# Performance work log

Measured on AMD Instinct MI355X. Metric: run time of the kernel, lower is better.

Reference implementation:

```python
import jax, jax.numpy as jnp
import numpy as np

WS = 14           # window_size
N = WS * WS       # tokens = 196
DIM = 768
H = 12
HD = DIM // H     # 64
B = 256
KSZ = 3


def make_local_mask():
    # True = masked out; 3x3 neighborhood around each query is kept (False)
    mask = np.ones((N, N), dtype=bool)
    for i in range(WS):
        for j in range(WS):
            cur = np.ones((WS, WS), dtype=bool)
            stx, sty = max(i - KSZ // 2, 0), max(j - KSZ // 2, 0)
            edx, edy = min(i + KSZ // 2, WS - 1), min(j + KSZ // 2, WS - 1)
            cur[stx:edx + 1, sty:edy + 1] = False
            mask[i * WS + j] = cur.reshape(-1)
    return mask


def make_rel_idx():
    coords = np.stack(np.meshgrid(np.arange(WS), np.arange(WS), indexing='ij'))  # [2,WS,WS]
    flat = coords.reshape(2, -1)                                                  # [2,N]
    rel = flat[:, :, None] - flat[:, None, :]                                     # [2,N,N]
    rel = rel.transpose(1, 2, 0).astype(np.int32)                                 # [N,N,2]
    rel[:, :, 0] += WS - 1
    rel[:, :, 1] += WS - 1
    rel[:, :, 0] *= 2 * WS - 1
    return rel.sum(-1)                                                            # [N,N] in [0, (2WS-1)^2)


def setup_inputs() -> dict:
    key = jax.random.key(0)
    ks = jax.random.split(key, 5)
    return {
        'x': jax.random.normal(ks[0], (B, N, DIM), jnp.float32),
        'w_qkv': jax.random.normal(ks[1], (3 * DIM, DIM), jnp.float32) * 0.02,
        'rpb_table': jax.random.normal(ks[2], ((2 * WS - 1) ** 2, H), jnp.float32) * 0.02,
        'proj_w': jax.random.normal(ks[3], (DIM, DIM), jnp.float32) * 0.02,
        'proj_b': jax.random.normal(ks[4], (DIM,), jnp.float32) * 0.02,
        'mask': jnp.asarray(make_local_mask()),
        'rel_idx': jnp.asarray(make_rel_idx()),
    }


def reference(x, w_qkv, rpb_table, proj_w, proj_b, mask, rel_idx):
    b, n, c = x.shape
    scale = HD ** -0.5
    qkv = x @ w_qkv.T                                   # [B,N,3*DIM]
    qkv = qkv.reshape(b, n, 3, H, HD).transpose(2, 0, 3, 1, 4)  # [3,B,H,N,HD]
    q, k, v = qkv[0] * scale, qkv[1], qkv[2]
    attn = jnp.einsum('bhqd,bhkd->bhqk', q, k)          # [B,H,N,N]
    neg = -jnp.finfo(attn.dtype).max
    attn = jnp.where(mask, neg, attn)
    # relative position bias gather: [N,N] indices into [T,H] -> [H,N,N]
    rpb = rpb_table[rel_idx].transpose(2, 0, 1)
    attn = attn + rpb[None]
    attn = jax.nn.softmax(attn, axis=-1)
    out = jnp.einsum('bhqk,bhkd->bhqd', attn, v)        # [B,H,N,HD]
    out = out.transpose(0, 2, 1, 3).reshape(b, n, H * HD)
    return out @ proj_w.T + proj_b
```

## Files before the change

kernel.cpp:

```cpp
#include <hip/hip_runtime.h>
#include <cstdint>
#include <cstddef>

typedef unsigned short u16;
typedef __attribute__((ext_vector_type(8))) short bf16x8;
typedef __attribute__((ext_vector_type(4))) float f32x4;

__device__ __forceinline__ u16 f2bf(float f) {
    unsigned u = __float_as_uint(f);
    u += 0x7FFF + ((u >> 16) & 1);
    return (u16)(u >> 16);
}
__device__ __forceinline__ float bf2f(u16 b) {
    return __uint_as_float(((unsigned)b) << 16);
}

__global__ __launch_bounds__(256) void cvt_bf16(const float4* __restrict__ in,
                                                u16* __restrict__ out, int n4) {
    int i = blockIdx.x * 256 + threadIdx.x;
    if (i >= n4) return;
    float4 v = in[i];
    ushort4 o;
    o.x = f2bf(v.x); o.y = f2bf(v.y); o.z = f2bf(v.z); o.w = f2bf(v.w);
    ((ushort4*)out)[i] = o;
}

__device__ __forceinline__ void gl_lds16(const u16* g, u16* l) {
    __builtin_amdgcn_global_load_lds(
        (const __attribute__((address_space(1))) void*)g,
        (__attribute__((address_space(3))) void*)l, 16, 0, 0);
}

#define MFMA16(a, b, c) __builtin_amdgcn_mfma_f32_16x16x32_bf16(a, b, c, 0, 0, 0)

__device__ __forceinline__ void BARRIER() {
    asm volatile("" ::: "memory");
    __builtin_amdgcn_s_barrier();
    asm volatile("" ::: "memory");
}
#define LGKM0() asm volatile("s_waitcnt lgkmcnt(0)" ::: "memory")

__device__ __forceinline__ bf16x8 lds_frag(const u16* base, int r, int c) {
    return *(const bf16x8*)((const char*)base + (r << 7) + ((c ^ (r & 7)) << 4));
}

__device__ __forceinline__ void stage_half(const u16* gbase, int K, u16* lbase,
                                           int kt, int h, int srow, int wuoff)
{
    const u16* gp = gbase + (size_t)(h * 128 + srow) * K + kt * 64;
    char* lp = (char*)lbase + h * 16384 + wuoff;
    gl_lds16(gp, (u16*)lp);
    gl_lds16(gp + (size_t)64 * K, (u16*)(lp + 8192));
}

template <bool IS_QKV>
__global__ __launch_bounds__(512, 2)
void gemm256(const u16* __restrict__ A, const u16* __restrict__ Bt,
             const float* __restrict__ bias, void* __restrict__ Cout,
             int M, int N, int K)
{
    __shared__ u16 As[2][16384];
    __shared__ u16 Bs[2][16384];

    const int tid = threadIdx.x;
    const int w   = tid >> 6;
    const int l   = tid & 63;
    const int wr  = w >> 2;
    const int wc  = w & 3;
    const int fr  = l & 15;
    const int ck0 = l >> 4;

    const int gx = gridDim.x;
    const int nwg = gx * gridDim.y;
    const int orig = blockIdx.y * gx + blockIdx.x;
    const int qq = nwg >> 3, rr = nwg & 7;
    const int xcd = orig & 7, idx = orig >> 3;
    const int wg = (xcd < rr) ? (xcd * (qq + 1) + idx)
                              : (rr * (qq + 1) + (xcd - rr) * qq + idx);
    const int bx = wg % gx, by = wg / gx;
    const int m0 = by * 256, n0 = bx * 256;

    const int srow   = w * 8 + (l >> 3);
    const int schunk = ((l & 7) ^ (l >> 3)) * 8;
    const int wuoff  = w * 1024;

    const u16* Ag = A  + (size_t)m0 * K + schunk;
    const u16* Bg = Bt + (size_t)n0 * K + schunk;

    f32x4 acc[8][4] = {};
    const int NT = K >> 6;

    stage_half(Ag, K, As[0], 0, 0, srow, wuoff);
    stage_half(Bg, K, Bs[0], 0, 0, srow, wuoff);
    stage_half(Ag, K, As[0], 0, 1, srow, wuoff);
    stage_half(Bg, K, Bs[0], 0, 1, srow, wuoff);
    stage_half(Ag, K, As[1], 1, 0, srow, wuoff);
    stage_half(Bg, K, Bs[1], 1, 0, srow, wuoff);
    asm volatile("s_waitcnt vmcnt(4)" ::: "memory");
    BARRIER();

    for (int g = 0; g < NT; ++g) {
        const u16* Ab = As[g & 1];
        const u16* Bb = Bs[g & 1];
        u16* Anx = As[(g + 1) & 1];
        u16* Bnx = Bs[(g + 1) & 1];
        u16* Acu = As[g & 1];
        u16* Bcu = Bs[g & 1];

        bf16x8 a0[8], a1[8], b0[4], b1[4];

        #pragma unroll
        for (int mi = 0; mi < 8; ++mi) a0[mi] = lds_frag(Ab, wr * 128 + mi * 16 + fr, ck0);
        b0[0] = lds_frag(Bb, wc * 64 + 0 * 16 + fr, ck0);
        b0[1] = lds_frag(Bb, wc * 64 + 1 * 16 + fr, ck0);
        if (g + 1 < NT) stage_half(Ag, K, Anx, g + 1, 1, srow, wuoff);
        BARRIER();
        LGKM0();
        __builtin_amdgcn_s_setprio(1);
        #pragma unroll
        for (int mi = 0; mi < 8; ++mi) {
            acc[mi][0] = MFMA16(a0[mi], b0[0], acc[mi][0]);
            acc[mi][1] = MFMA16(a0[mi], b0[1], acc[mi][1]);
        }
        __builtin_amdgcn_s_setprio(0);
        BARRIER();

        b0[2] = lds_frag(Bb, wc * 64 + 2 * 16 + fr, ck0);
        b0[3] = lds_frag(Bb, wc * 64 + 3 * 16 + fr, ck0);
        #pragma unroll
        for (int mi = 0; mi < 8; ++mi) a1[mi] = lds_frag(Ab, wr * 128 + mi * 16 + fr, ck0 + 4);
        #pragma unroll
        for (int ni = 0; ni < 4; ++ni) b1[ni] = lds_frag(Bb, wc * 64 + ni * 16 + fr, ck0 + 4);
        if (g + 1 < NT) stage_half(Bg, K, Bnx, g + 1, 1, srow, wuoff);
        BARRIER();
        LGKM0();
        __builtin_amdgcn_s_setprio(1);
        #pragma unroll
        for (int mi = 0; mi < 8; ++mi) {
            acc[mi][2] = MFMA16(a0[mi], b0[2], acc[mi][2]);
            acc[mi][3] = MFMA16(a0[mi], b0[3], acc[mi][3]);
        }
        __builtin_amdgcn_s_setprio(0);
        BARRIER();

        if (g + 2 < NT) stage_half(Ag, K, Acu, g + 2, 0, srow, wuoff);
        BARRIER();
        __builtin_amdgcn_s_setprio(1);
        #pragma unroll
        for (int mi = 0; mi < 8; ++mi) {
            acc[mi][0] = MFMA16(a1[mi], b1[0], acc[mi][0]);
            acc[mi][1] = MFMA16(a1[mi], b1[1], acc[mi][1]);
        }
        __builtin_amdgcn_s_setprio(0);
        BARRIER();

        if (g + 2 < NT) stage_half(Bg, K, Bcu, g + 2, 0, srow, wuoff);
        __builtin_amdgcn_s_setprio(1);
        #pragma unroll
        for (int mi = 0; mi < 8; ++mi) {
            acc[mi][2] = MFMA16(a1[mi], b1[2], acc[mi][2]);
            acc[mi][3] = MFMA16(a1[mi], b1[3], acc[mi][3]);
        }
        __builtin_amdgcn_s_setprio(0);
        if (g < NT - 2) { asm volatile("s_waitcnt vmcnt(4)" ::: "memory"); }
        else            { asm volatile("s_waitcnt vmcnt(0)" ::: "memory"); }
        BARRIER();
    }

    if (IS_QKV) {
        u16* C = (u16*)Cout;
        #pragma unroll
        for (int mi = 0; mi < 8; ++mi) {
            const int r0 = m0 + wr * 128 + mi * 16 + (l >> 4) * 4;
            #pragma unroll
            for (int ni = 0; ni < 4; ++ni) {
                const int col = n0 + wc * 64 + ni * 16 + fr;
                const float sc = (col < 768) ? 0.125f : 1.0f;
                #pragma unroll
                for (int r = 0; r < 4; ++r)
                    C[(size_t)(r0 + r) * N + col] = f2bf(acc[mi][ni][r] * sc);
            }
        }
    } else {
        float* C = (float*)Cout;
        #pragma unroll
        for (int mi = 0; mi < 8; ++mi) {
            const int r0 = m0 + wr * 128 + mi * 16 + (l >> 4) * 4;
            #pragma unroll
            for (int ni = 0; ni < 4; ++ni) {
                const int col = n0 + wc * 64 + ni * 16 + fr;
                const float b = bias[col];
                #pragma unroll
                for (int r = 0; r < 4; ++r)
                    C[(size_t)(r0 + r) * N + col] = acc[mi][ni][r] + b;
            }
        }
    }
}

__device__ __forceinline__ void load_bf8(const u16* p, float* f) {
    uint4 d = *(const uint4*)p;
    f[0] = __uint_as_float(d.x << 16); f[1] = __uint_as_float(d.x & 0xFFFF0000u);
    f[2] = __uint_as_float(d.y << 16); f[3] = __uint_as_float(d.y & 0xFFFF0000u);
    f[4] = __uint_as_float(d.z << 16); f[5] = __uint_as_float(d.z & 0xFFFF0000u);
    f[6] = __uint_as_float(d.w << 16); f[7] = __uint_as_float(d.w & 0xFFFF0000u);
}

__global__ __launch_bounds__(256)
void attn_sparse2(const u16* __restrict__ qkv, const float* __restrict__ rpb,
                  u16* __restrict__ out)
{
    const int lane = threadIdx.x & 63;
    const int wid  = blockIdx.x * 4 + (threadIdx.x >> 6);
    const int sub  = lane >> 3;
    const int sl   = lane & 7;
    const int gq   = wid * 8 + sub;
    const int bt   = gq / 12;
    const int h    = gq - bt * 12;
    const int t    = bt % 196;
    const int i    = t / 14, j = t % 14;

    const size_t rowbase = (size_t)(bt - t) * 2304 + h * 64 + sl * 8;

    float qf[8];
    load_bf8(qkv + (size_t)bt * 2304 + h * 64 + sl * 8, qf);

    float s[9];
    int   t2a[9];
    #pragma unroll
    for (int di = -1; di <= 1; ++di) {
        #pragma unroll
        for (int dj = -1; dj <= 1; ++dj) {
            const int idx = (di + 1) * 3 + (dj + 1);
            const int i2 = i + di, j2 = j + dj;
            const bool valid = ((unsigned)i2 < 14u) && ((unsigned)j2 < 14u);
            const int t2 = valid ? (i2 * 14 + j2) : t;
            t2a[idx] = t2;
            float kf[8];
            load_bf8(qkv + rowbase + (size_t)t2 * 2304 + 768, kf);
            float p = qf[0] * kf[0];
            #pragma unroll
            for (int d = 1; d < 8; ++d) p = fmaf(qf[d], kf[d], p);
            p += __shfl_xor(p, 1);
            p += __shfl_xor(p, 2);
            p += __shfl_xor(p, 4);
            const int ridx = (13 - di) * 27 + (13 - dj);
            s[idx] = valid ? (p + rpb[ridx * 12 + h]) : -1e30f;
        }
    }
    float mx = s[0];
    #pragma unroll
    for (int a = 1; a < 9; ++a) mx = fmaxf(mx, s[a]);

    float den = 0.f, o[8] = {};
    #pragma unroll
    for (int a = 0; a < 9; ++a) {
        float vf[8];
        load_bf8(qkv + rowbase + (size_t)t2a[a] * 2304 + 1536, vf);
        const float p = __expf(s[a] - mx);
        den += p;
        #pragma unroll
        for (int d = 0; d < 8; ++d) o[d] = fmaf(p, vf[d], o[d]);
    }
    const float r = 1.0f / den;
    ushort4 o0, o1;
    o0.x = f2bf(o[0] * r); o0.y = f2bf(o[1] * r);
    o0.z = f2bf(o[2] * r); o0.w = f2bf(o[3] * r);
    o1.x = f2bf(o[4] * r); o1.y = f2bf(o[5] * r);
    o1.z = f2bf(o[6] * r); o1.w = f2bf(o[7] * r);
    u16* op = out + (size_t)bt * 768 + h * 64 + sl * 8;
    *(ushort4*)op = o0;
    *(ushort4*)(op + 4) = o1;
}

extern "C" void kernel_launch(void* const* d_in, const int* in_sizes, int n_in,
                              void* d_out, int out_size, void* d_ws, size_t ws_size,
                              hipStream_t stream)
{
    const float* x      = (const float*)d_in[0];
    const float* w_qkv  = (const float*)d_in[1];
    const float* rpb    = (const float*)d_in[2];
    const float* proj_w = (const float*)d_in[3];
    const float* proj_b = (const float*)d_in[4];
    float* out = (float*)d_out;

    char* ws = (char*)d_ws;
    u16* x_bf    = (u16*)(ws);
    u16* wqkv_bf = (u16*)(ws + 77070336ULL);
    u16* pw_bf   = (u16*)(ws + 80609280ULL);
    u16* qkv_bf  = (u16*)(ws + 81788928ULL);
    u16* attn_bf = (u16*)(ws + 312999936ULL);

    cvt_bf16<<<37632, 256, 0, stream>>>((const float4*)x,      x_bf,    9633792);
    cvt_bf16<<<1728,  256, 0, stream>>>((const float4*)w_qkv,  wqkv_bf, 442368);
    cvt_bf16<<<576,   256, 0, stream>>>((const float4*)proj_w, pw_bf,   147456);

    gemm256<true><<<dim3(9, 196), 512, 0, stream>>>(
        x_bf, wqkv_bf, nullptr, qkv_bf, 50176, 2304, 768);

    attn_sparse2<<<18816, 256, 0, stream>>>(qkv_bf, rpb, attn_bf);

    gemm256<false><<<dim3(3, 196), 512, 0, stream>>>(
        attn_bf, pw_bf, proj_b, out, 50176, 768, 768);
}
```

Measured before the change: 703.6 us.

## Stage K/V per batch-head in LDS for attention; restructure GEMM prefetch into whole tiles

The attention kernel now launches one block per (batch, head). Each block loads all 196 K and V rows for that head into swizzled LDS once and computes every query's 3x3 neighbourhood from LDS, instead of re-reading neighbour rows from global memory for each query. The GEMM prefetch now issues a whole A/B tile two iterations ahead at a single point, replacing the split half-tile staging, and adjusts the vmcnt waits to match. The trade-offs are fewer attention blocks with more LDS per block, and less interleaving of loads with MFMA work in the GEMM.

```diff
diff --git a/kernel.cpp b/kernel.cpp
--- a/kernel.cpp
+++ b/kernel.cpp
@@ -10,9 +10,6 @@
     unsigned u = __float_as_uint(f);
     u += 0x7FFF + ((u >> 16) & 1);
     return (u16)(u >> 16);
-}
-__device__ __forceinline__ float bf2f(u16 b) {
-    return __uint_as_float(((unsigned)b) << 16);
 }
 
 __global__ __launch_bounds__(256) void cvt_bf16(const float4* __restrict__ in,
@@ -51,6 +48,16 @@
     char* lp = (char*)lbase + h * 16384 + wuoff;
     gl_lds16(gp, (u16*)lp);
     gl_lds16(gp + (size_t)64 * K, (u16*)(lp + 8192));
+}
+
+__device__ __forceinline__ void stage_tile(const u16* Ag, const u16* Bg, int K,
+                                           u16* Ab, u16* Bb, int kt,
+                                           int srow, int wuoff)
+{
+    stage_half(Ag, K, Ab, kt, 0, srow, wuoff);
+    stage_half(Ag, K, Ab, kt, 1, srow, wuoff);
+    stage_half(Bg, K, Bb, kt, 0, srow, wuoff);
+    stage_half(Bg, K, Bb, kt, 1, srow, wuoff);
 }
 
 template <bool IS_QKV>
@@ -90,20 +97,14 @@
     f32x4 acc[8][4] = {};
     const int NT = K >> 6;
 
-    stage_half(Ag, K, As[0], 0, 0, srow, wuoff);
-    stage_half(Bg, K, Bs[0], 0, 0, srow, wuoff);
-    stage_half(Ag, K, As[0], 0, 1, srow, wuoff);
-    stage_half(Bg, K, Bs[0], 0, 1, srow, wuoff);
-    stage_half(Ag, K, As[1], 1, 0, srow, wuoff);
-    stage_half(Bg, K, Bs[1], 1, 0, srow, wuoff);
-    asm volatile("s_waitcnt vmcnt(4)" ::: "memory");
+    stage_tile(Ag, Bg, K, As[0], Bs[0], 0, srow, wuoff);
+    stage_tile(Ag, Bg, K, As[1], Bs[1], 1, srow, wuoff);
+    asm volatile("s_waitcnt vmcnt(8)" ::: "memory");
     BARRIER();
 
     for (int g = 0; g < NT; ++g) {
         const u16* Ab = As[g & 1];
         const u16* Bb = Bs[g & 1];
-        u16* Anx = As[(g + 1) & 1];
-        u16* Bnx = Bs[(g + 1) & 1];
         u16* Acu = As[g & 1];
         u16* Bcu = Bs[g & 1];
 
@@ -113,7 +114,6 @@
         for (int mi = 0; mi < 8; ++mi) a0[mi] = lds_frag(Ab, wr * 128 + mi * 16 + fr, ck0);
         b0[0] = lds_frag(Bb, wc * 64 + 0 * 16 + fr, ck0);
         b0[1] = lds_frag(Bb, wc * 64 + 1 * 16 + fr, ck0);
-        if (g + 1 < NT) stage_half(Ag, K, Anx, g + 1, 1, srow, wuoff);
         BARRIER();
         LGKM0();
         __builtin_amdgcn_s_setprio(1);
@@ -131,7 +131,6 @@
         for (int mi = 0; mi < 8; ++mi) a1[mi] = lds_frag(Ab, wr * 128 + mi * 16 + fr, ck0 + 4);
         #pragma unroll
         for (int ni = 0; ni < 4; ++ni) b1[ni] = lds_frag(Bb, wc * 64 + ni * 16 + fr, ck0 + 4);
-        if (g + 1 < NT) stage_half(Bg, K, Bnx, g + 1, 1, srow, wuoff);
         BARRIER();
         LGKM0();
         __builtin_amdgcn_s_setprio(1);
@@ -143,7 +142,7 @@
         __builtin_amdgcn_s_setprio(0);
         BARRIER();
 
-        if (g + 2 < NT) stage_half(Ag, K, Acu, g + 2, 0, srow, wuoff);
+        if (g + 2 < NT) stage_tile(Ag, Bg, K, Acu, Bcu, g + 2, srow, wuoff);
         BARRIER();
         __builtin_amdgcn_s_setprio(1);
         #pragma unroll
@@ -154,7 +153,6 @@
         __builtin_amdgcn_s_setprio(0);
         BARRIER();
 
-        if (g + 2 < NT) stage_half(Bg, K, Bcu, g + 2, 0, srow, wuoff);
         __builtin_amdgcn_s_setprio(1);
         #pragma unroll
         for (int mi = 0; mi < 8; ++mi) {
@@ -162,7 +160,7 @@
             acc[mi][3] = MFMA16(a1[mi], b1[3], acc[mi][3]);
         }
         __builtin_amdgcn_s_setprio(0);
-        if (g < NT - 2) { asm volatile("s_waitcnt vmcnt(4)" ::: "memory"); }
+        if (g < NT - 2) { asm volatile("s_waitcnt vmcnt(8)" ::: "memory"); }
         else            { asm volatile("s_waitcnt vmcnt(0)" ::: "memory"); }
         BARRIER();
     }
@@ -198,8 +196,7 @@
     }
 }
 
-__device__ __forceinline__ void load_bf8(const u16* p, float* f) {
-    uint4 d = *(const uint4*)p;
+__device__ __forceinline__ void unpack8(uint4 d, float* f) {
     f[0] = __uint_as_float(d.x << 16); f[1] = __uint_as_float(d.x & 0xFFFF0000u);
     f[2] = __uint_as_float(d.y << 16); f[3] = __uint_as_float(d.y & 0xFFFF0000u);
     f[4] = __uint_as_float(d.z << 16); f[5] = __uint_as_float(d.z & 0xFFFF0000u);
@@ -207,70 +204,96 @@
 }
 
 __global__ __launch_bounds__(256)
-void attn_sparse2(const u16* __restrict__ qkv, const float* __restrict__ rpb,
-                  u16* __restrict__ out)
-{
-    const int lane = threadIdx.x & 63;
-    const int wid  = blockIdx.x * 4 + (threadIdx.x >> 6);
-    const int sub  = lane >> 3;
-    const int sl   = lane & 7;
-    const int gq   = wid * 8 + sub;
-    const int bt   = gq / 12;
-    const int h    = gq - bt * 12;
-    const int t    = bt % 196;
-    const int i    = t / 14, j = t % 14;
-
-    const size_t rowbase = (size_t)(bt - t) * 2304 + h * 64 + sl * 8;
-
-    float qf[8];
-    load_bf8(qkv + (size_t)bt * 2304 + h * 64 + sl * 8, qf);
-
-    float s[9];
-    int   t2a[9];
+void attn_lds(const u16* __restrict__ qkv, const float* __restrict__ rpb,
+              u16* __restrict__ out)
+{
+    __shared__ u16 Ks[196 * 64];
+    __shared__ u16 Vs[196 * 64];
+
+    const int tid = threadIdx.x;
+    const int bh  = blockIdx.x;
+    const int b   = bh / 12;
+    const int h   = bh - b * 12;
+    const size_t base = (size_t)b * 196 * 2304 + h * 64;
+
+    for (int c = tid; c < 1568; c += 256) {
+        const int t = c >> 3, s = c & 7;
+        const u16* kg = qkv + base + (size_t)t * 2304 + 768 + s * 8;
+        uint4 kd = *(const uint4*)kg;
+        uint4 vd = *(const uint4*)(kg + 768);
+        const int off = t * 64 + ((s * 8) ^ ((t & 7) << 3));
+        *(uint4*)&Ks[off] = kd;
+        *(uint4*)&Vs[off] = vd;
+    }
+
+    float rpb9[9];
     #pragma unroll
-    for (int di = -1; di <= 1; ++di) {
-        #pragma unroll
-        for (int dj = -1; dj <= 1; ++dj) {
-            const int idx = (di + 1) * 3 + (dj + 1);
+    for (int a = 0; a < 9; ++a) {
+        const int di = a / 3 - 1, dj = a % 3 - 1;
+        rpb9[a] = rpb[((13 - di) * 27 + (13 - dj)) * 12 + h];
+    }
+
+    __syncthreads();
+
+    const int w   = tid >> 6;
+    const int sub = (tid >> 3) & 7;
+    const int sl  = tid & 7;
+
+    for (int p = 0; p < 7; ++p) {
+        const int t = p * 32 + w * 8 + sub;
+        const bool qv = t < 196;
+        const int tt = qv ? t : 195;
+        const int i = tt / 14, j = tt % 14;
+
+        float qf[8];
+        unpack8(*(const uint4*)(qkv + base + (size_t)tt * 2304 + sl * 8), qf);
+
+        float s[9];
+        int   t2a[9];
+        #pragma unroll
+        for (int a = 0; a < 9; ++a) {
+            const int di = a / 3 - 1, dj = a % 3 - 1;
             const int i2 = i + di, j2 = j + dj;
             const bool valid = ((unsigned)i2 < 14u) && ((unsigned)j2 < 14u);
-            const int t2 = valid ? (i2 * 14 + j2) : t;
-            t2a[idx] = t2;
+            const int t2 = valid ? (i2 * 14 + j2) : tt;
+            t2a[a] = t2;
             float kf[8];
-            load_bf8(qkv + rowbase + (size_t)t2 * 2304 + 768, kf);
-            float p = qf[0] * kf[0];
+            unpack8(*(const uint4*)&Ks[t2 * 64 + ((sl * 8) ^ ((t2 & 7) << 3))], kf);
+            float pp = qf[0] * kf[0];
             #pragma unroll
-            for (int d = 1; d < 8; ++d) p = fmaf(qf[d], kf[d], p);
-            p += __shfl_xor(p, 1);
-            p += __shfl_xor(p, 2);
-            p += __shfl_xor(p, 4);
-            const int ridx = (13 - di) * 27 + (13 - dj);
-            s[idx] = valid ? (p + rpb[ridx * 12 + h]) : -1e30f;
-        }
-    }
-    float mx = s[0];
-    #pragma unroll
-    for (int a = 1; a < 9; ++a) mx = fmaxf(mx, s[a]);
-
-    float den = 0.f, o[8] = {};
-    #pragma unroll
-    for (int a = 0; a < 9; ++a) {
-        float vf[8];
-        load_bf8(qkv + rowbase + (size_t)t2a[a] * 2304 + 1536, vf);
-        const float p = __expf(s[a] - mx);
-        den += p;
-        #pragma unroll
-        for (int d = 0; d < 8; ++d) o[d] = fmaf(p, vf[d], o[d]);
-    }
-    const float r = 1.0f / den;
-    ushort4 o0, o1;
-    o0.x = f2bf(o[0] * r); o0.y = f2bf(o[1] * r);
-    o0.z = f2bf(o[2] * r); o0.w = f2bf(o[3] * r);
-    o1.x = f2bf(o[4] * r); o1.y = f2bf(o[5] * r);
-    o1.z = f2bf(o[6] * r); o1.w = f2bf(o[7] * r);
-    u16* op = out + (size_t)bt * 768 + h * 64 + sl * 8;
-    *(ushort4*)op = o0;
-    *(ushort4*)(op + 4) = o1;
+            for (int d = 1; d < 8; ++d) pp = fmaf(qf[d], kf[d], pp);
+            pp += __shfl_xor(pp, 1);
+            pp += __shfl_xor(pp, 2);
+            pp += __shfl_xor(pp, 4);
+            s[a] = valid ? (pp + rpb9[a]) : -1e30f;
+        }
+        float mx = s[0];
+        #pragma unroll
+        for (int a = 1; a < 9; ++a) mx = fmaxf(mx, s[a]);
+
+        float den = 0.f, o[8] = {};
+        #pragma unroll
+        for (int a = 0; a < 9; ++a) {
+            float vf[8];
+            const int t2 = t2a[a];
+            unpack8(*(const uint4*)&Vs[t2 * 64 + ((sl * 8) ^ ((t2 & 7) << 3))], vf);
+            const float pe = __expf(s[a] - mx);
+            den += pe;
+            #pragma unroll
+            for (int d = 0; d < 8; ++d) o[d] = fmaf(pe, vf[d], o[d]);
+        }
+        const float r = 1.0f / den;
+        if (qv) {
+            ushort4 o0, o1;
+            o0.x = f2bf(o[0] * r); o0.y = f2bf(o[1] * r);
+            o0.z = f2bf(o[2] * r); o0.w = f2bf(o[3] * r);
+            o1.x = f2bf(o[4] * r); o1.y = f2bf(o[5] * r);
+            o1.z = f2bf(o[6] * r); o1.w = f2bf(o[7] * r);
+            u16* op = out + (size_t)(b * 196 + t) * 768 + h * 64 + sl * 8;
+            *(ushort4*)op = o0;
+            *(ushort4*)(op + 4) = o1;
+        }
+    }
 }
 
 extern "C" void kernel_launch(void* const* d_in, const int* in_sizes, int n_in,
@@ -298,7 +321,7 @@
     gemm256<true><<<dim3(9, 196), 512, 0, stream>>>(
         x_bf, wqkv_bf, nullptr, qkv_bf, 50176, 2304, 768);
 
-    attn_sparse2<<<18816, 256, 0, stream>>>(qkv_bf, rpb, attn_bf);
+    attn_lds<<<3072, 256, 0, stream>>>(qkv_bf, rpb, attn_bf);
 
     gemm256<false><<<dim3(3, 196), 512, 0, stream>>>(
         attn_bf, pw_bf, proj_b, out, 50176, 768, 768);
```

Result: faster. 686.9 us (-2.4%).
